# Optimization experiments

Hardware: AMD Instinct MI355X
Metric: run time of the kernel (lower is better)

## Reference

```python
import jax, jax.numpy as jnp
import numpy as np

B, H, N, D = 4, 8, 2048, 64  # d_model=512, n_heads=8 -> d_head=64
MASK_PROB = 0.1
SCALE = D ** -0.5


def setup_inputs() -> dict:
    key = jax.random.key(0)
    kq, kk, kv, km = jax.random.split(key, 4)
    q = jax.random.normal(kq, (B, H, N, D), dtype=jnp.float32)
    k = jax.random.normal(kk, (B, H, N, D), dtype=jnp.float32)
    v = jax.random.normal(kv, (B, H, N, D), dtype=jnp.float32)
    # torch.bernoulli(full(..., prob)): 1 with prob=mask_prob -> dropped
    mask = jax.random.bernoulli(km, MASK_PROB, (B, H, N, N))
    return {"q": q, "k": k, "v": v, "mask": mask}


def reference(q, k, v, mask):
    # [B,H,N,N] scores: QK^T * scale -> tanh -> zero where mask is True
    scores = jnp.tanh(jnp.einsum("bhnd,bhmd->bhnm", q, k) * SCALE)
    scores = scores * (~mask).astype(scores.dtype)
    return jnp.einsum("bhnm,bhmd->bhnd", scores, v)
```

## Files before the change

### kernel.cpp

```cpp
#include <hip/hip_runtime.h>

namespace {

constexpr int N = 2048;
constexpr int D = 64;
constexpr float SCALE = 0.125f;
constexpr int LK = 72;
constexpr int LV = 68;
constexpr int NT = N / 64;

typedef __attribute__((ext_vector_type(8))) short bf16x8;
typedef __attribute__((ext_vector_type(4))) short short4v;
typedef __attribute__((ext_vector_type(4))) float f32x4;
typedef __attribute__((ext_vector_type(4))) int   int4v;

__device__ inline short f2bf(float x) {
  union { float f; unsigned u; } a; a.f = x;
  unsigned r = a.u + 0x7fffu + ((a.u >> 16) & 1u);
  return (short)(r >> 16);
}

__device__ inline float fast_tanh(float x) {
  float e = __builtin_amdgcn_exp2f(x * 2.885390081777927f);
  return 1.0f - 2.0f * __builtin_amdgcn_rcpf(e + 1.0f);
}

}

__global__ __launch_bounds__(256) void attn_tanh_kernel(
    const float* __restrict__ Q, const float* __restrict__ K,
    const float* __restrict__ V, const int* __restrict__ M,
    float* __restrict__ O)
{
  __shared__ __align__(16) short k_s[64 * LK];
  __shared__ __align__(16) short s_s[64 * LK];
  __shared__ __align__(16) short vt_s[64 * LV];

  const int tid  = threadIdx.x;
  const int wave = tid >> 6;
  const int lane = tid & 63;
  const int l15  = lane & 15;
  const int quad = lane >> 4;

  const int bh = blockIdx.x >> 5;
  const int q0 = (blockIdx.x & 31) * 64;

  const float* qp = Q + (size_t)bh * N * D;
  const float* kp = K + (size_t)bh * N * D;
  const float* vp = V + (size_t)bh * N * D;
  const int*   mp = M + (size_t)bh * N * N;
  float* op = O + (size_t)bh * N * D;

  bf16x8 qf[2];
  {
    const float* qrow = qp + (size_t)(q0 + wave * 16 + l15) * D + quad * 8;
#pragma unroll
    for (int ks = 0; ks < 2; ++ks) {
      float4 f0 = *(const float4*)(qrow + ks * 32);
      float4 f1 = *(const float4*)(qrow + ks * 32 + 4);
      bf16x8 t;
      t[0] = f2bf(f0.x); t[1] = f2bf(f0.y); t[2] = f2bf(f0.z); t[3] = f2bf(f0.w);
      t[4] = f2bf(f1.x); t[5] = f2bf(f1.y); t[6] = f2bf(f1.z); t[7] = f2bf(f1.w);
      qf[ks] = t;
    }
  }

  const int r0 = tid >> 4;
  const int c4 = (tid & 15) << 2;

  float4 kreg[4];
  float  vreg[16];
  int4v  mreg[4];

  const float* vbase = vp + (size_t)(wave * 16) * D + lane;
  const int*   mbase = mp + (size_t)(q0 + wave * 16 + l15) * N + quad * 4;

#pragma unroll
  for (int i = 0; i < 4; ++i)
    kreg[i] = *(const float4*)(kp + (size_t)(i * 16 + r0) * D + c4);
#pragma unroll
  for (int i = 0; i < 16; ++i)
    vreg[i] = vbase[(size_t)i * D];
#pragma unroll
  for (int ct = 0; ct < 4; ++ct)
    mreg[ct] = __builtin_nontemporal_load((const int4v*)(mbase + ct * 16));

  f32x4 o_acc[4];
#pragma unroll
  for (int i = 0; i < 4; ++i) o_acc[i] = (f32x4){0.f, 0.f, 0.f, 0.f};

  for (int kt = 0; kt < NT; ++kt) {
    __syncthreads();

#pragma unroll
    for (int i = 0; i < 4; ++i) {
      short4v kv;
      kv[0] = f2bf(kreg[i].x); kv[1] = f2bf(kreg[i].y);
      kv[2] = f2bf(kreg[i].z); kv[3] = f2bf(kreg[i].w);
      *(short4v*)(&k_s[(i * 16 + r0) * LK + c4]) = kv;
    }
#pragma unroll
    for (int c = 0; c < 4; ++c) {
      short4v vv;
      vv[0] = f2bf(vreg[4 * c + 0]); vv[1] = f2bf(vreg[4 * c + 1]);
      vv[2] = f2bf(vreg[4 * c + 2]); vv[3] = f2bf(vreg[4 * c + 3]);
      *(short4v*)(&vt_s[lane * LV + wave * 16 + 4 * c]) = vv;
    }
    __syncthreads();

#pragma unroll
    for (int ct = 0; ct < 4; ++ct) {
      f32x4 acc = {0.f, 0.f, 0.f, 0.f};
#pragma unroll
      for (int ks = 0; ks < 2; ++ks) {
        bf16x8 a = *(const bf16x8*)(&k_s[(ct * 16 + l15) * LK + ks * 32 + quad * 8]);
        acc = __builtin_amdgcn_mfma_f32_16x16x32_bf16(a, qf[ks], acc, 0, 0, 0);
      }
      short4v sv;
#pragma unroll
      for (int r = 0; r < 4; ++r) {
        float s = fast_tanh(acc[r] * SCALE);
        sv[r] = mreg[ct][r] ? (short)0 : f2bf(s);
      }
      *(short4v*)(&s_s[(wave * 16 + l15) * LK + ct * 16 + quad * 4]) = sv;
    }

    if (kt + 1 < NT) {
      const float* kpt = kp + (size_t)(kt + 1) * 64 * D;
#pragma unroll
      for (int i = 0; i < 4; ++i)
        kreg[i] = *(const float4*)(kpt + (size_t)(i * 16 + r0) * D + c4);
      const float* vpt = vbase + (size_t)(kt + 1) * 64 * D;
#pragma unroll
      for (int i = 0; i < 16; ++i)
        vreg[i] = vpt[(size_t)i * D];
      const int* mb = mbase + (size_t)(kt + 1) * 64;
#pragma unroll
      for (int ct = 0; ct < 4; ++ct)
        mreg[ct] = __builtin_nontemporal_load((const int4v*)(mb + ct * 16));
    }

#pragma unroll
    for (int ks = 0; ks < 2; ++ks) {
      bf16x8 a = *(const bf16x8*)(&s_s[(wave * 16 + l15) * LK + ks * 32 + quad * 8]);
#pragma unroll
      for (int nt = 0; nt < 4; ++nt) {
        const short* vb = &vt_s[(nt * 16 + l15) * LV + ks * 32 + quad * 8];
        short4v lo = *(const short4v*)(vb);
        short4v hi = *(const short4v*)(vb + 4);
        bf16x8 b = __builtin_shufflevector(lo, hi, 0, 1, 2, 3, 4, 5, 6, 7);
        o_acc[nt] = __builtin_amdgcn_mfma_f32_16x16x32_bf16(a, b, o_acc[nt], 0, 0, 0);
      }
    }
  }

#pragma unroll
  for (int nt = 0; nt < 4; ++nt) {
#pragma unroll
    for (int r = 0; r < 4; ++r) {
      op[(q0 + wave * 16 + quad * 4 + r) * D + nt * 16 + l15] = o_acc[nt][r];
    }
  }
}

extern "C" void kernel_launch(void* const* d_in, const int* in_sizes, int n_in,
                              void* d_out, int out_size, void* d_ws, size_t ws_size,
                              hipStream_t stream) {
  const float* q = (const float*)d_in[0];
  const float* k = (const float*)d_in[1];
  const float* v = (const float*)d_in[2];
  const int* m = (const int*)d_in[3];
  float* out = (float*)d_out;

  attn_tanh_kernel<<<dim3(1024), dim3(256), 0, stream>>>(q, k, v, m, out);
}
```

Before: 758.5 us.

## Double-buffer K/V shared tiles and use packed bf16 conversions

Splits the K and V shared-memory tiles into two buffers and unrolls the key loop by two. The next tile's global loads are issued and its conversion to LDS overlaps compute on the current buffer, which removes one barrier per tile. All fp32-to-bf16 conversions now go through the hardware packed cvt builtin when it is available, falling back to the manual rounding otherwise. The cost is extra LDS and register pressure from the duplicated staging registers, which may reduce occupancy.

```diff
diff --git a/kernel.cpp b/kernel.cpp
--- a/kernel.cpp
+++ b/kernel.cpp
@@ -11,6 +11,7 @@
 
 typedef __attribute__((ext_vector_type(8))) short bf16x8;
 typedef __attribute__((ext_vector_type(4))) short short4v;
+typedef __attribute__((ext_vector_type(2))) short short2v;
 typedef __attribute__((ext_vector_type(4))) float f32x4;
 typedef __attribute__((ext_vector_type(4))) int   int4v;
 
@@ -18,6 +19,24 @@
   union { float f; unsigned u; } a; a.f = x;
   unsigned r = a.u + 0x7fffu + ((a.u >> 16) & 1u);
   return (short)(r >> 16);
+}
+
+#if __has_builtin(__builtin_amdgcn_cvt_pk_bf16_f32)
+typedef __attribute__((ext_vector_type(2))) __bf16 bfv2;
+__device__ inline short2v pk_bf(float lo, float hi) {
+  bfv2 t = __builtin_amdgcn_cvt_pk_bf16_f32(lo, hi);
+  return __builtin_bit_cast(short2v, t);
+}
+#else
+__device__ inline short2v pk_bf(float lo, float hi) {
+  short2v r; r[0] = f2bf(lo); r[1] = f2bf(hi); return r;
+}
+#endif
+
+__device__ inline short4v pk4(float4 f) {
+  short2v a = pk_bf(f.x, f.y), b = pk_bf(f.z, f.w);
+  short4v r; r[0] = a[0]; r[1] = a[1]; r[2] = b[0]; r[3] = b[1];
+  return r;
 }
 
 __device__ inline float fast_tanh(float x) {
@@ -32,9 +51,9 @@
     const float* __restrict__ V, const int* __restrict__ M,
     float* __restrict__ O)
 {
-  __shared__ __align__(16) short k_s[64 * LK];
+  __shared__ __align__(16) short k_s[2][64 * LK];
+  __shared__ __align__(16) short vt_s[2][64 * LV];
   __shared__ __align__(16) short s_s[64 * LK];
-  __shared__ __align__(16) short vt_s[64 * LV];
 
   const int tid  = threadIdx.x;
   const int wave = tid >> 6;
@@ -58,9 +77,10 @@
     for (int ks = 0; ks < 2; ++ks) {
       float4 f0 = *(const float4*)(qrow + ks * 32);
       float4 f1 = *(const float4*)(qrow + ks * 32 + 4);
+      short4v lo = pk4(f0), hi = pk4(f1);
       bf16x8 t;
-      t[0] = f2bf(f0.x); t[1] = f2bf(f0.y); t[2] = f2bf(f0.z); t[3] = f2bf(f0.w);
-      t[4] = f2bf(f1.x); t[5] = f2bf(f1.y); t[6] = f2bf(f1.z); t[7] = f2bf(f1.w);
+      t[0]=lo[0]; t[1]=lo[1]; t[2]=lo[2]; t[3]=lo[3];
+      t[4]=hi[0]; t[5]=hi[1]; t[6]=hi[2]; t[7]=hi[3];
       qf[ks] = t;
     }
   }
@@ -68,90 +88,91 @@
   const int r0 = tid >> 4;
   const int c4 = (tid & 15) << 2;
 
-  float4 kreg[4];
-  float  vreg[16];
-  int4v  mreg[4];
-
   const float* vbase = vp + (size_t)(wave * 16) * D + lane;
   const int*   mbase = mp + (size_t)(q0 + wave * 16 + l15) * N + quad * 4;
 
+  float4 kA[4], kB[4];
+  float  vA[16], vB[16];
+  int4v  mA[4], mB[4];
+
+  auto issue_loads = [&](int kt1, float4* kr, float* vr, int4v* mr) {
+    const float* kpt = kp + (size_t)kt1 * 64 * D;
 #pragma unroll
-  for (int i = 0; i < 4; ++i)
-    kreg[i] = *(const float4*)(kp + (size_t)(i * 16 + r0) * D + c4);
+    for (int i = 0; i < 4; ++i)
+      kr[i] = *(const float4*)(kpt + (size_t)(i * 16 + r0) * D + c4);
+    const float* vpt = vbase + (size_t)kt1 * 64 * D;
 #pragma unroll
-  for (int i = 0; i < 16; ++i)
-    vreg[i] = vbase[(size_t)i * D];
+    for (int i = 0; i < 16; ++i)
+      vr[i] = vpt[(size_t)i * D];
+    const int* mb = mbase + (size_t)kt1 * 64;
 #pragma unroll
-  for (int ct = 0; ct < 4; ++ct)
-    mreg[ct] = __builtin_nontemporal_load((const int4v*)(mbase + ct * 16));
+    for (int ct = 0; ct < 4; ++ct)
+      mr[ct] = __builtin_nontemporal_load((const int4v*)(mb + ct * 16));
+  };
+
+  auto write_kv = [&](int buf, const float4* kr, const float* vr) {
+#pragma unroll
+    for (int i = 0; i < 4; ++i)
+      *(short4v*)(&k_s[buf][(i * 16 + r0) * LK + c4]) = pk4(kr[i]);
+#pragma unroll
+    for (int c = 0; c < 4; ++c) {
+      short2v p0 = pk_bf(vr[4 * c + 0], vr[4 * c + 1]);
+      short2v p1 = pk_bf(vr[4 * c + 2], vr[4 * c + 3]);
+      short4v vv; vv[0] = p0[0]; vv[1] = p0[1]; vv[2] = p1[0]; vv[3] = p1[1];
+      *(short4v*)(&vt_s[buf][lane * LV + wave * 16 + 4 * c]) = vv;
+    }
+  };
 
   f32x4 o_acc[4];
 #pragma unroll
   for (int i = 0; i < 4; ++i) o_acc[i] = (f32x4){0.f, 0.f, 0.f, 0.f};
 
-  for (int kt = 0; kt < NT; ++kt) {
-    __syncthreads();
-
-#pragma unroll
-    for (int i = 0; i < 4; ++i) {
-      short4v kv;
-      kv[0] = f2bf(kreg[i].x); kv[1] = f2bf(kreg[i].y);
-      kv[2] = f2bf(kreg[i].z); kv[3] = f2bf(kreg[i].w);
-      *(short4v*)(&k_s[(i * 16 + r0) * LK + c4]) = kv;
-    }
-#pragma unroll
-    for (int c = 0; c < 4; ++c) {
-      short4v vv;
-      vv[0] = f2bf(vreg[4 * c + 0]); vv[1] = f2bf(vreg[4 * c + 1]);
-      vv[2] = f2bf(vreg[4 * c + 2]); vv[3] = f2bf(vreg[4 * c + 3]);
-      *(short4v*)(&vt_s[lane * LV + wave * 16 + 4 * c]) = vv;
-    }
-    __syncthreads();
-
+  auto compute = [&](int buf, const int4v* mr) {
+    const short* ks_ = k_s[buf];
+    const short* vs_ = vt_s[buf];
 #pragma unroll
     for (int ct = 0; ct < 4; ++ct) {
       f32x4 acc = {0.f, 0.f, 0.f, 0.f};
 #pragma unroll
-      for (int ks = 0; ks < 2; ++ks) {
-        bf16x8 a = *(const bf16x8*)(&k_s[(ct * 16 + l15) * LK + ks * 32 + quad * 8]);
-        acc = __builtin_amdgcn_mfma_f32_16x16x32_bf16(a, qf[ks], acc, 0, 0, 0);
+      for (int ksi = 0; ksi < 2; ++ksi) {
+        bf16x8 a = *(const bf16x8*)(&ks_[(ct * 16 + l15) * LK + ksi * 32 + quad * 8]);
+        acc = __builtin_amdgcn_mfma_f32_16x16x32_bf16(a, qf[ksi], acc, 0, 0, 0);
       }
-      short4v sv;
-#pragma unroll
-      for (int r = 0; r < 4; ++r) {
-        float s = fast_tanh(acc[r] * SCALE);
-        sv[r] = mreg[ct][r] ? (short)0 : f2bf(s);
-      }
+      float s0 = mr[ct][0] ? 0.f : fast_tanh(acc[0] * SCALE);
+      float s1 = mr[ct][1] ? 0.f : fast_tanh(acc[1] * SCALE);
+      float s2 = mr[ct][2] ? 0.f : fast_tanh(acc[2] * SCALE);
+      float s3 = mr[ct][3] ? 0.f : fast_tanh(acc[3] * SCALE);
+      short2v p0 = pk_bf(s0, s1), p1 = pk_bf(s2, s3);
+      short4v sv; sv[0] = p0[0]; sv[1] = p0[1]; sv[2] = p1[0]; sv[3] = p1[1];
       *(short4v*)(&s_s[(wave * 16 + l15) * LK + ct * 16 + quad * 4]) = sv;
     }
-
-    if (kt + 1 < NT) {
-      const float* kpt = kp + (size_t)(kt + 1) * 64 * D;
 #pragma unroll
-      for (int i = 0; i < 4; ++i)
-        kreg[i] = *(const float4*)(kpt + (size_t)(i * 16 + r0) * D + c4);
-      const float* vpt = vbase + (size_t)(kt + 1) * 64 * D;
-#pragma unroll
-      for (int i = 0; i < 16; ++i)
-        vreg[i] = vpt[(size_t)i * D];
-      const int* mb = mbase + (size_t)(kt + 1) * 64;
-#pragma unroll
-      for (int ct = 0; ct < 4; ++ct)
-        mreg[ct] = __builtin_nontemporal_load((const int4v*)(mb + ct * 16));
-    }
-
-#pragma unroll
-    for (int ks = 0; ks < 2; ++ks) {
-      bf16x8 a = *(const bf16x8*)(&s_s[(wave * 16 + l15) * LK + ks * 32 + quad * 8]);
+    for (int ksi = 0; ksi < 2; ++ksi) {
+      bf16x8 a = *(const bf16x8*)(&s_s[(wave * 16 + l15) * LK + ksi * 32 + quad * 8]);
 #pragma unroll
       for (int nt = 0; nt < 4; ++nt) {
-        const short* vb = &vt_s[(nt * 16 + l15) * LV + ks * 32 + quad * 8];
+        const short* vb = &vs_[(nt * 16 + l15) * LV + ksi * 32 + quad * 8];
         short4v lo = *(const short4v*)(vb);
         short4v hi = *(const short4v*)(vb + 4);
         bf16x8 b = __builtin_shufflevector(lo, hi, 0, 1, 2, 3, 4, 5, 6, 7);
         o_acc[nt] = __builtin_amdgcn_mfma_f32_16x16x32_bf16(a, b, o_acc[nt], 0, 0, 0);
       }
     }
+  };
+
+  issue_loads(0, kA, vA, mA);
+  write_kv(0, kA, vA);
+
+  for (int kt = 0; kt < NT; kt += 2) {
+    __syncthreads();
+    issue_loads(kt + 1, kB, vB, mB);
+    compute(0, mA);
+    write_kv(1, kB, vB);
+
+    __syncthreads();
+    if (kt + 2 < NT) issue_loads(kt + 2, kA, vA, mA);
+    compute(1, mB);
+    if (kt + 2 < NT) write_kv(0, kA, vA);
   }
 
 #pragma unroll
```

Result: no change. 771.1 us (+1.7%).
